# Kernel tuning notes

Hardware: AMD Instinct MI355X
Metric: run time of the kernel (lower is better)

## Reference

```python
import jax, jax.numpy as jnp
import numpy as np

B, S, D, H = 2, 2048, 2048, 16
DK = D // H


def setup_inputs() -> dict:
    key = jax.random.key(0)
    k1, k2, k3 = jax.random.split(key, 3)
    x = jax.random.normal(k1, (B, S, D), dtype=jnp.float32)
    # trunc-normal in the original; plain normal with matching std is fine for a numeric baseline
    std_qkv = 2.0 / (DK + D)  # note: original passes variance as std to trunc_normal_
    W_qkv = jax.random.normal(k2, (3 * D, D), dtype=jnp.float32) * std_qkv
    W_o = jax.random.normal(k3, (D, D), dtype=jnp.float32) * (1.0 / D)
    return {"x": x, "W_qkv": W_qkv, "W_o": W_o}


def reference(x, W_qkv, W_o):
    b, s, d = x.shape
    # fused QKV projection: y = x @ W_qkv^T
    qkv = jnp.einsum('bsd,ed->bse', x, W_qkv)  # [b, s, 3d]
    q, k, v = jnp.split(qkv, 3, axis=-1)
    # [b, s, d] -> [b, h, s, dk]
    def to_heads(t):
        return t.reshape(b, s, H, DK).transpose(0, 2, 1, 3)
    q, k, v = to_heads(q), to_heads(k), to_heads(v)
    scores = jnp.einsum('bhqd,bhkd->bhqk', q, k) / np.sqrt(DK).astype(np.float32)
    causal = jnp.tril(jnp.ones((s, s), dtype=bool))
    scores = jnp.where(causal, scores, -jnp.inf)
    att = jax.nn.softmax(scores, axis=-1)
    out = jnp.einsum('bhqk,bhkd->bhqd', att, v)  # [b, h, s, dk]
    out = out.transpose(0, 2, 1, 3).reshape(b, s, d)
    return jnp.einsum('bsd,od->bso', out, W_o)
```

## Files before the change

kernel.cpp:

```cpp
#include <hip/hip_runtime.h>

typedef _Float16 f16;
typedef _Float16 f16x4 __attribute__((ext_vector_type(4)));
typedef _Float16 f16x8 __attribute__((ext_vector_type(8)));
typedef float    f32x4 __attribute__((ext_vector_type(4)));

#define MFMA_F16(a,b,c) __builtin_amdgcn_mfma_f32_16x16x32_f16((a),(b),(c),0,0,0)

static constexpr int B_  = 2;
static constexpr int S_  = 2048;
static constexpr int D_  = 2048;
static constexpr int H_  = 16;
static constexpr int DK_ = 128;
static constexpr int K_  = 2048;

__device__ __forceinline__ void gload_lds16(const void* g, void* l) {
  __builtin_amdgcn_global_load_lds(
      (const __attribute__((address_space(1))) void*)g,
      (__attribute__((address_space(3))) void*)l, 16, 0, 0);
}

__global__ __launch_bounds__(256) void cast_all_kernel(const float* __restrict__ x,
                                                       const float* __restrict__ wqkv,
                                                       const float* __restrict__ wo,
                                                       f16* __restrict__ xb,
                                                       f16* __restrict__ wqkvb,
                                                       f16* __restrict__ wob) {
  const int total = 6291456;
  int i = blockIdx.x * 256 + threadIdx.x;
  int stride = gridDim.x * 256;
  for (int j = i; j < total; j += stride) {
    const float* src; f16* dst; int jj;
    if (j < 2097152)      { src = x;    dst = xb;    jj = j; }
    else if (j < 5242880) { src = wqkv; dst = wqkvb; jj = j - 2097152; }
    else                  { src = wo;   dst = wob;   jj = j - 5242880; }
    float4 v = reinterpret_cast<const float4*>(src)[jj];
    f16x4 o = {(f16)v.x, (f16)v.y, (f16)v.z, (f16)v.w};
    reinterpret_cast<f16x4*>(dst)[jj] = o;
  }
}


#define SYNCW0                                          \
  asm volatile("s_waitcnt vmcnt(0)" ::: "memory");      \
  __builtin_amdgcn_s_barrier();                         \
  asm volatile("" ::: "memory");

__device__ __forceinline__ void stage2(const f16* gA, const f16* gB, char* slot, int w) {
  gload_lds16(gA,      slot +         w * 1024);
  gload_lds16(gA + 32, slot +  8192 + w * 1024);
  gload_lds16(gB,      slot + 16384 + w * 1024);
  gload_lds16(gB + 32, slot + 24576 + w * 1024);
}

__device__ __forceinline__ void compute2(const char* slot, int aoff, int boff, int lro,
                                         f32x4 (&acc)[4][2]) {
  f16x8 a0[4], b0[2], a1[4], b1[2];
#pragma unroll
  for (int mi = 0; mi < 4; ++mi) {
    a0[mi] = *(const f16x8*)(slot +        aoff + mi * 1024 + lro);
    a1[mi] = *(const f16x8*)(slot + 8192 + aoff + mi * 1024 + lro);
  }
#pragma unroll
  for (int ni = 0; ni < 2; ++ni) {
    b0[ni] = *(const f16x8*)(slot + 16384 + boff + ni * 1024 + lro);
    b1[ni] = *(const f16x8*)(slot + 24576 + boff + ni * 1024 + lro);
  }
  __builtin_amdgcn_s_setprio(1);
#pragma unroll
  for (int mi = 0; mi < 4; ++mi)
#pragma unroll
    for (int ni = 0; ni < 2; ++ni)
      acc[mi][ni] = MFMA_F16(a0[mi], b0[ni], acc[mi][ni]);
#pragma unroll
  for (int mi = 0; mi < 4; ++mi)
#pragma unroll
    for (int ni = 0; ni < 2; ++ni)
      acc[mi][ni] = MFMA_F16(a1[mi], b1[ni], acc[mi][ni]);
  __builtin_amdgcn_s_setprio(0);
}

__device__ __forceinline__ void gemm_core_db(const f16* __restrict__ A,
                                             const f16* __restrict__ Bw,
                                             int brow, int bcol, char* lds,
                                             f32x4 (&acc)[4][2]) {
  const int tid = threadIdx.x;
  const int w = tid >> 6, l = tid & 63;
  const int lg = l >> 4, lr = l & 15;
  const int wm = w >> 2, wn = w & 3;
  const int lro = (lr * 4 + (lg ^ ((lr >> 1) & 3))) * 16;
  const int aoff = wm * 4096;
  const int boff = wn * 2048;

#pragma unroll
  for (int mi = 0; mi < 4; ++mi)
#pragma unroll
    for (int ni = 0; ni < 2; ++ni) acc[mi][ni] = (f32x4){0.f, 0.f, 0.f, 0.f};

  const int kgsrc = (l & 3) ^ ((l >> 3) & 3);
  const f16* gA = A  + (size_t)(brow * 128 + w * 16 + (l >> 2)) * K_ + kgsrc * 8;
  const f16* gB = Bw + (size_t)(bcol * 128 + w * 16 + (l >> 2)) * K_ + kgsrc * 8;

  char* s0 = lds;
  char* s1 = lds + 32768;

  stage2(gA, gB, s0, w);
  SYNCW0

  for (int tb = 0; tb < 16; ++tb) {
    const int t = tb * 2;
    stage2(gA + (size_t)(t + 1) * 64, gB + (size_t)(t + 1) * 64, s1, w);
    compute2(s0, aoff, boff, lro, acc);
    SYNCW0
    if (tb < 15)
      stage2(gA + (size_t)(t + 2) * 64, gB + (size_t)(t + 2) * 64, s0, w);
    compute2(s1, aoff, boff, lro, acc);
    SYNCW0
  }
}

__global__ __launch_bounds__(512, 4) void gemm_qkv_kernel(const f16* __restrict__ xb,
                                                          const f16* __restrict__ wqkv,
                                                          f16* __restrict__ Q,
                                                          f16* __restrict__ Kk,
                                                          f16* __restrict__ Vt) {
  __shared__ __align__(16) char lds[65536];
  const int bid = blockIdx.x;
  const int xcd = bid & 7;
  const int local = bid >> 3;
  const int brow = xcd * 4 + (local & 3);
  const int bcol = local >> 2;

  f32x4 acc[4][2];
  gemm_core_db(xb, wqkv, brow, bcol, lds, acc);

  const int tid = threadIdx.x;
  const int w = tid >> 6, l = tid & 63;
  const int lg = l >> 4, lr = l & 15;
  const int wm = w >> 2, wn = w & 3;

  const int which = bcol >> 4;
  const int h = bcol & 15;

  if (which == 2) {
#pragma unroll
    for (int mi = 0; mi < 4; ++mi) {
      const int m0 = brow * 128 + wm * 64 + mi * 16 + lg * 4;
      const int b = m0 >> 11, s = m0 & 2047;
#pragma unroll
      for (int ni = 0; ni < 2; ++ni) {
        const int dk = wn * 32 + ni * 16 + lr;
        f16x4 v = {(f16)acc[mi][ni][0], (f16)acc[mi][ni][1],
                   (f16)acc[mi][ni][2], (f16)acc[mi][ni][3]};
        *(f16x4*)(Vt + ((size_t)(b * H_ + h) * DK_ + dk) * S_ + s) = v;
      }
    }
  } else {
    f16* outp = (which == 0) ? Q : Kk;
    const float scale = (which == 0) ? 0.08838834764831845f : 1.0f;
#pragma unroll
    for (int mi = 0; mi < 4; ++mi) {
      const int m0 = brow * 128 + wm * 64 + mi * 16 + lg * 4;
#pragma unroll
      for (int ni = 0; ni < 2; ++ni) {
        const int dk = wn * 32 + ni * 16 + lr;
#pragma unroll
        for (int r = 0; r < 4; ++r) {
          const int mm = m0 + r;
          const int b = mm >> 11, s = mm & 2047;
          outp[(((size_t)b * H_ + h) * S_ + s) * DK_ + dk] = (f16)(acc[mi][ni][r] * scale);
        }
      }
    }
  }
}

__global__ __launch_bounds__(512, 4) void gemm_out_kernel(const f16* __restrict__ ab,
                                                          const f16* __restrict__ wo,
                                                          float* __restrict__ out) {
  __shared__ __align__(16) char lds[65536];
  const int bid = blockIdx.x;
  const int xcd = bid & 7;
  const int local = bid >> 3;
  const int brow = xcd * 4 + (local & 3);
  const int bcol = local >> 2;

  f32x4 acc[4][2];
  gemm_core_db(ab, wo, brow, bcol, lds, acc);

  const int tid = threadIdx.x;
  const int w = tid >> 6, l = tid & 63;
  const int lg = l >> 4, lr = l & 15;
  const int wm = w >> 2, wn = w & 3;

#pragma unroll
  for (int mi = 0; mi < 4; ++mi) {
    const int m0 = brow * 128 + wm * 64 + mi * 16 + lg * 4;
#pragma unroll
    for (int ni = 0; ni < 2; ++ni) {
      const int n = bcol * 128 + wn * 32 + ni * 16 + lr;
#pragma unroll
      for (int r = 0; r < 4; ++r)
        out[(size_t)(m0 + r) * D_ + n] = acc[mi][ni][r];
    }
  }
}

__global__ __launch_bounds__(256) void attn_kernel(const f16* __restrict__ Q,
                                                   const f16* __restrict__ Kg,
                                                   const f16* __restrict__ Vt,
                                                   f16* __restrict__ O) {
  __shared__ __align__(16) unsigned char Ks[64 * 256];
  __shared__ __align__(16) unsigned char Vs[128 * 128];
  __shared__ __align__(16) unsigned char Ps[4][16 * 128];

  const int bid = blockIdx.x;
  const int pr = bid & 15;
  const int h  = (bid >> 4) & 15;
  const int b  = bid >> 8;
  const int bh = b * H_ + h;
  const int tid = threadIdx.x;
  const int w = tid >> 6, l = tid & 63;
  const int lg = l >> 4, lr = l & 15;

  for (int half = 0; half < 2; ++half) {
    const int qt = half ? (31 - pr) : pr;

    const f16* Qg = Q + ((size_t)bh * S_ + qt * 64 + w * 16) * DK_;
    f16x8 qf[4];
#pragma unroll
    for (int kd = 0; kd < 4; ++kd)
      qf[kd] = *(const f16x8*)(Qg + (size_t)lr * DK_ + kd * 32 + lg * 8);

    f32x4 o[8];
#pragma unroll
    for (int n = 0; n < 8; ++n) o[n] = (f32x4){0.f, 0.f, 0.f, 0.f};
    float mrun[4] = {-1e30f, -1e30f, -1e30f, -1e30f};
    float lrun[4] = {0.f, 0.f, 0.f, 0.f};

    const int ntiles = qt + 1;
    for (int kt = 0; kt < ntiles; ++kt) {
      __syncthreads();
      const f16* Kt = Kg + ((size_t)bh * S_ + kt * 64) * DK_;
#pragma unroll
      for (int i = 0; i < 4; ++i) {
        const int chunk = i * 256 + tid;
        const int row = chunk >> 4, c8 = chunk & 15;
        uint4 v = *(const uint4*)(Kt + (size_t)row * DK_ + c8 * 8);
        *(uint4*)(Ks + row * 256 + ((c8 * 16) ^ ((row & 7) << 4))) = v;
      }
      const f16* Vtt = Vt + (size_t)bh * DK_ * S_ + kt * 64;
#pragma unroll
      for (int i = 0; i < 4; ++i) {
        const int chunk = i * 256 + tid;
        const int row = chunk >> 3, c8 = chunk & 7;
        uint4 v = *(const uint4*)(Vtt + (size_t)row * S_ + c8 * 8);
        *(uint4*)(Vs + row * 128 + ((c8 * 16) ^ ((row & 7) << 4))) = v;
      }
      __syncthreads();

      f32x4 s[4];
#pragma unroll
      for (int j = 0; j < 4; ++j) s[j] = (f32x4){0.f, 0.f, 0.f, 0.f};
      __builtin_amdgcn_s_setprio(1);
#pragma unroll
      for (int j = 0; j < 4; ++j) {
        const int row = j * 16 + lr;
#pragma unroll
        for (int kd = 0; kd < 4; ++kd) {
          f16x8 kf = *(const f16x8*)(Ks + row * 256 + ((kd * 64 + lg * 16) ^ ((row & 7) << 4)));
          s[j] = MFMA_F16(qf[kd], kf, s[j]);
        }
      }
      __builtin_amdgcn_s_setprio(0);
      if (kt == qt) {
#pragma unroll
        for (int j = 0; j < 4; ++j) {
          const int col = j * 16 + lr;
#pragma unroll
          for (int r = 0; r < 4; ++r) {
            const int qrow = w * 16 + lg * 4 + r;
            if (col > qrow) s[j][r] = -1e30f;
          }
        }
      }
      float scl[4];
#pragma unroll
      for (int r = 0; r < 4; ++r) {
        float m0 = fmaxf(fmaxf(s[0][r], s[1][r]), fmaxf(s[2][r], s[3][r]));
#pragma unroll
        for (int msk = 1; msk < 16; msk <<= 1) m0 = fmaxf(m0, __shfl_xor(m0, msk, 64));
        const float nm = fmaxf(mrun[r], m0);
        scl[r] = __expf(mrun[r] - nm);
        mrun[r] = nm;
      }
      float rs[4] = {0.f, 0.f, 0.f, 0.f};
#pragma unroll
      for (int j = 0; j < 4; ++j) {
#pragma unroll
        for (int r = 0; r < 4; ++r) {
          const float p = __expf(fmaxf(s[j][r] - mrun[r], -80.f));
          rs[r] += p;
          const int row = lg * 4 + r;
          const int cb = (j * 16 + lr) * 2;
          *(f16*)(Ps[w] + row * 128 + (cb ^ ((row & 7) << 4))) = (f16)p;
        }
      }
#pragma unroll
      for (int r = 0; r < 4; ++r) {
        float t = rs[r];
#pragma unroll
        for (int msk = 1; msk < 16; msk <<= 1) t += __shfl_xor(t, msk, 64);
        lrun[r] = lrun[r] * scl[r] + t;
      }
#pragma unroll
      for (int n = 0; n < 8; ++n)
#pragma unroll
        for (int r = 0; r < 4; ++r) o[n][r] *= scl[r];

      asm volatile("s_waitcnt lgkmcnt(0)" ::: "memory");

      __builtin_amdgcn_s_setprio(1);
#pragma unroll
      for (int ks = 0; ks < 2; ++ks) {
        f16x8 pf = *(const f16x8*)(Ps[w] + lr * 128 + ((ks * 64 + lg * 16) ^ ((lr & 7) << 4)));
#pragma unroll
        for (int n = 0; n < 8; ++n) {
          const int row = n * 16 + lr;
          f16x8 vf = *(const f16x8*)(Vs + row * 128 + ((ks * 64 + lg * 16) ^ ((row & 7) << 4)));
          o[n] = MFMA_F16(pf, vf, o[n]);
        }
      }
      __builtin_amdgcn_s_setprio(0);
    }

#pragma unroll
    for (int r = 0; r < 4; ++r) {
      const float inv = 1.0f / lrun[r];
      const int srow = qt * 64 + w * 16 + lg * 4 + r;
      f16* op = O + ((size_t)b * S_ + srow) * D_ + h * DK_;
#pragma unroll
      for (int n = 0; n < 8; ++n) op[n * 16 + lr] = (f16)(o[n][r] * inv);
    }
  }
}

extern "C" void kernel_launch(void* const* d_in, const int* in_sizes, int n_in,
                              void* d_out, int out_size, void* d_ws, size_t ws_size,
                              hipStream_t stream) {
  const float* x    = (const float*)d_in[0];
  const float* wqkv = (const float*)d_in[1];
  const float* wo   = (const float*)d_in[2];
  float* out = (float*)d_out;
  char* ws = (char*)d_ws;

  f16* xb     = (f16*)(ws + 0);
  f16* wqkvb  = (f16*)(ws + 16777216);
  f16* wob    = (f16*)(ws + 41943040);
  f16* Qb     = (f16*)(ws + 50331648);
  f16* Kb     = (f16*)(ws + 67108864);
  f16* Vtb    = (f16*)(ws + 83886080);
  f16* attn_o = (f16*)(ws + 0);

  cast_all_kernel<<<2048, 256, 0, stream>>>(x, wqkv, wo, xb, wqkvb, wob);

  gemm_qkv_kernel<<<1536, 512, 0, stream>>>(xb, wqkvb, Qb, Kb, Vtb);
  attn_kernel<<<512, 256, 0, stream>>>(Qb, Kb, Vtb, attn_o);
  gemm_out_kernel<<<512, 512, 0, stream>>>(attn_o, wob, out);
}
```

Before: 264.1 us.

## Double-buffer K/V tiles with async global-to-LDS loads in attention kernel

Replaces the synchronous register-staged K/V tile loads in the attention kernel with direct global_load_lds transfers into double-buffered LDS, prefetching the next tile while the current one is computed. LDS layout changes to 1KB sub-tile blocks with an XOR swizzle chosen so the MFMA fragment reads stay conflict-free. The point is to hide global memory latency behind the QK and PV MFMAs. In exchange LDS use roughly doubles, which may reduce occupancy, and correctness now relies on hand-placed vmcnt waits and barriers.

```diff
diff --git a/kernel.cpp b/kernel.cpp
--- a/kernel.cpp
+++ b/kernel.cpp
@@ -210,9 +210,9 @@
                                                    const f16* __restrict__ Kg,
                                                    const f16* __restrict__ Vt,
                                                    f16* __restrict__ O) {
-  __shared__ __align__(16) unsigned char Ks[64 * 256];
-  __shared__ __align__(16) unsigned char Vs[128 * 128];
-  __shared__ __align__(16) unsigned char Ps[4][16 * 128];
+  __shared__ __align__(16) char Kbuf2[2][16384];
+  __shared__ __align__(16) char Vbuf2[2][16384];
+  __shared__ __align__(16) unsigned char Ps[4][2048];
 
   const int bid = blockIdx.x;
   const int pr = bid & 15;
@@ -222,6 +222,12 @@
   const int tid = threadIdx.x;
   const int w = tid >> 6, l = tid & 63;
   const int lg = l >> 4, lr = l & 15;
+  const int lrow = l >> 2;
+  const int kgsrc = (l & 3) ^ ((l >> 3) & 3);
+  const int lro = (lr * 4 + (lg ^ ((lr >> 1) & 3))) * 16;
+
+  const f16* Kbase = Kg + (size_t)bh * S_ * DK_;
+  const f16* Vbase = Vt + (size_t)bh * DK_ * S_;
 
   for (int half = 0; half < 2; ++half) {
     const int qt = half ? (31 - pr) : pr;
@@ -239,25 +245,51 @@
     float lrun[4] = {0.f, 0.f, 0.f, 0.f};
 
     const int ntiles = qt + 1;
+
+    {
+      const f16* Kt = Kbase;
+      const f16* Vp = Vbase;
+#pragma unroll
+      for (int i = 0; i < 4; ++i) {
+        const int u = w * 4 + i;
+        gload_lds16(Kt + (size_t)((u >> 2) * 16 + lrow) * DK_ + (u & 3) * 32 + kgsrc * 8,
+                    Kbuf2[0] + u * 1024);
+      }
+#pragma unroll
+      for (int i = 0; i < 4; ++i) {
+        const int u = w * 4 + i;
+        gload_lds16(Vp + (size_t)((u >> 1) * 16 + lrow) * S_ + (u & 1) * 32 + kgsrc * 8,
+                    Vbuf2[0] + u * 1024);
+      }
+    }
+
     for (int kt = 0; kt < ntiles; ++kt) {
-      __syncthreads();
-      const f16* Kt = Kg + ((size_t)bh * S_ + kt * 64) * DK_;
-#pragma unroll
-      for (int i = 0; i < 4; ++i) {
-        const int chunk = i * 256 + tid;
-        const int row = chunk >> 4, c8 = chunk & 15;
-        uint4 v = *(const uint4*)(Kt + (size_t)row * DK_ + c8 * 8);
-        *(uint4*)(Ks + row * 256 + ((c8 * 16) ^ ((row & 7) << 4))) = v;
-      }
-      const f16* Vtt = Vt + (size_t)bh * DK_ * S_ + kt * 64;
-#pragma unroll
-      for (int i = 0; i < 4; ++i) {
-        const int chunk = i * 256 + tid;
-        const int row = chunk >> 3, c8 = chunk & 7;
-        uint4 v = *(const uint4*)(Vtt + (size_t)row * S_ + c8 * 8);
-        *(uint4*)(Vs + row * 128 + ((c8 * 16) ^ ((row & 7) << 4))) = v;
-      }
-      __syncthreads();
+      const int cur = kt & 1;
+      if (kt + 1 < ntiles) {
+        const f16* Kt = Kbase + (size_t)(kt + 1) * 64 * DK_;
+        const f16* Vp = Vbase + (kt + 1) * 64;
+        char* Kb = Kbuf2[cur ^ 1];
+        char* Vb = Vbuf2[cur ^ 1];
+#pragma unroll
+        for (int i = 0; i < 4; ++i) {
+          const int u = w * 4 + i;
+          gload_lds16(Kt + (size_t)((u >> 2) * 16 + lrow) * DK_ + (u & 3) * 32 + kgsrc * 8,
+                      Kb + u * 1024);
+        }
+#pragma unroll
+        for (int i = 0; i < 4; ++i) {
+          const int u = w * 4 + i;
+          gload_lds16(Vp + (size_t)((u >> 1) * 16 + lrow) * S_ + (u & 1) * 32 + kgsrc * 8,
+                      Vb + u * 1024);
+        }
+        asm volatile("s_waitcnt vmcnt(8)" ::: "memory");
+      } else {
+        asm volatile("s_waitcnt vmcnt(0)" ::: "memory");
+      }
+      __builtin_amdgcn_s_barrier();
+
+      const char* Kb = Kbuf2[cur];
+      const char* Vb = Vbuf2[cur];
 
       f32x4 s[4];
 #pragma unroll
@@ -265,10 +297,9 @@
       __builtin_amdgcn_s_setprio(1);
 #pragma unroll
       for (int j = 0; j < 4; ++j) {
-        const int row = j * 16 + lr;
 #pragma unroll
         for (int kd = 0; kd < 4; ++kd) {
-          f16x8 kf = *(const f16x8*)(Ks + row * 256 + ((kd * 64 + lg * 16) ^ ((row & 7) << 4)));
+          f16x8 kf = *(const f16x8*)(Kb + ((j << 2) + kd) * 1024 + lro);
           s[j] = MFMA_F16(qf[kd], kf, s[j]);
         }
       }
@@ -326,12 +357,12 @@
         f16x8 pf = *(const f16x8*)(Ps[w] + lr * 128 + ((ks * 64 + lg * 16) ^ ((lr & 7) << 4)));
 #pragma unroll
         for (int n = 0; n < 8; ++n) {
-          const int row = n * 16 + lr;
-          f16x8 vf = *(const f16x8*)(Vs + row * 128 + ((ks * 64 + lg * 16) ^ ((row & 7) << 4)));
+          f16x8 vf = *(const f16x8*)(Vb + ((n << 1) + ks) * 1024 + lro);
           o[n] = MFMA_F16(pf, vf, o[n]);
         }
       }
       __builtin_amdgcn_s_setprio(0);
+      __builtin_amdgcn_s_barrier();
     }
 
 #pragma unroll
```

New measurement: 266.9 us. About the same (+1.1%).

## Rewrite QKV GEMM with 128x256 tiles and triple-buffered K=32 pipeline

Applied to the files above, without the earlier changes.

Replaces the shared double-buffered QKV GEMM core with a dedicated kernel that uses 128x256 output tiles (each wave holds a 4x4 MFMA accumulator block) and halves the grid to 768 blocks. The K loop now stages 32-wide slices into three rotating LDS buffers and waits with a partial vmcnt, so more loads stay in flight across barriers. It also raises MFMA priority during compute. The larger tile is meant to improve operand reuse and cut global/LDS traffic per FLOP, at the cost of more registers, lower occupancy (the min-blocks launch bound is dropped) and fewer blocks to spread across CUs.

```diff
diff --git a/kernel.cpp b/kernel.cpp
--- a/kernel.cpp
+++ b/kernel.cpp
@@ -41,6 +41,126 @@
 }
 
 
+__device__ __forceinline__ void qkv_stage(const f16* pA, const f16* pB0, const f16* pB1,
+                                          int t, char* slot, int w) {
+  gload_lds16(pA  + t * 32, slot +         w * 1024);
+  gload_lds16(pB0 + t * 32, slot +  8192 + w * 1024);
+  gload_lds16(pB1 + t * 32, slot +  8192 + (w + 8) * 1024);
+}
+
+__device__ __forceinline__ void qkv_compute(const char* slot, int aoff, int boff, int lro,
+                                            f32x4 (&acc)[4][4]) {
+  f16x8 af[4], bf[4];
+#pragma unroll
+  for (int mi = 0; mi < 4; ++mi)
+    af[mi] = *(const f16x8*)(slot + aoff + mi * 1024 + lro);
+#pragma unroll
+  for (int ni = 0; ni < 4; ++ni)
+    bf[ni] = *(const f16x8*)(slot + 8192 + boff + ni * 1024 + lro);
+  __builtin_amdgcn_s_setprio(1);
+#pragma unroll
+  for (int mi = 0; mi < 4; ++mi)
+#pragma unroll
+    for (int ni = 0; ni < 4; ++ni)
+      acc[mi][ni] = MFMA_F16(af[mi], bf[ni], acc[mi][ni]);
+  __builtin_amdgcn_s_setprio(0);
+}
+
+#define QKV_SYNC(N)                                           \
+  asm volatile("s_waitcnt vmcnt(" #N ")" ::: "memory");       \
+  __builtin_amdgcn_s_barrier();                               \
+  asm volatile("" ::: "memory");
+
+__global__ __launch_bounds__(512) void gemm_qkv_kernel(const f16* __restrict__ xb,
+                                                       const f16* __restrict__ wqkv,
+                                                       f16* __restrict__ Q,
+                                                       f16* __restrict__ Kk,
+                                                       f16* __restrict__ Vt) {
+  __shared__ __align__(16) char lds[73728];
+  const int bid = blockIdx.x;
+  const int xcd = bid & 7;
+  const int local = bid >> 3;
+  const int brow = xcd * 4 + (local & 3);
+  const int bcol = local >> 2;
+
+  const int tid = threadIdx.x;
+  const int w = tid >> 6, l = tid & 63;
+  const int lg = l >> 4, lr = l & 15;
+  const int wm = w >> 2, wn = w & 3;
+  const int lro = (lr * 4 + (lg ^ ((lr >> 1) & 3))) * 16;
+  const int aoff = wm * 4096;
+  const int boff = wn * 4096;
+
+  f32x4 acc[4][4];
+#pragma unroll
+  for (int mi = 0; mi < 4; ++mi)
+#pragma unroll
+    for (int ni = 0; ni < 4; ++ni) acc[mi][ni] = (f32x4){0.f, 0.f, 0.f, 0.f};
+
+  const int lrow = l >> 2;
+  const int kgsrc = (l & 3) ^ ((l >> 3) & 3);
+  const f16* pA  = xb   + (size_t)(brow * 128 + w * 16 + lrow) * K_ + kgsrc * 8;
+  const f16* pB0 = wqkv + (size_t)(bcol * 256 + w * 16 + lrow) * K_ + kgsrc * 8;
+  const f16* pB1 = wqkv + (size_t)(bcol * 256 + (w + 8) * 16 + lrow) * K_ + kgsrc * 8;
+
+  char* s0 = lds;
+  char* s1 = lds + 24576;
+  char* s2 = lds + 49152;
+
+  qkv_stage(pA, pB0, pB1, 0, s0, w);
+  qkv_stage(pA, pB0, pB1, 1, s1, w);
+  QKV_SYNC(3)
+
+  for (int tb = 0; tb < 20; ++tb) {
+    const int t = 3 * tb;
+    qkv_stage(pA, pB0, pB1, t + 2, s2, w); qkv_compute(s0, aoff, boff, lro, acc); QKV_SYNC(3)
+    qkv_stage(pA, pB0, pB1, t + 3, s0, w); qkv_compute(s1, aoff, boff, lro, acc); QKV_SYNC(3)
+    qkv_stage(pA, pB0, pB1, t + 4, s1, w); qkv_compute(s2, aoff, boff, lro, acc); QKV_SYNC(3)
+  }
+  qkv_stage(pA, pB0, pB1, 62, s2, w); qkv_compute(s0, aoff, boff, lro, acc); QKV_SYNC(3)
+  qkv_stage(pA, pB0, pB1, 63, s0, w); qkv_compute(s1, aoff, boff, lro, acc); QKV_SYNC(3)
+  qkv_compute(s2, aoff, boff, lro, acc);
+  QKV_SYNC(0)
+  qkv_compute(s0, aoff, boff, lro, acc);
+
+  const int which = bcol >> 3;
+  const int nbase = (bcol & 7) * 256 + wn * 64;
+
+  if (which == 2) {
+#pragma unroll
+    for (int mi = 0; mi < 4; ++mi) {
+      const int m0 = brow * 128 + wm * 64 + mi * 16 + lg * 4;
+      const int b = m0 >> 11, s = m0 & 2047;
+#pragma unroll
+      for (int ni = 0; ni < 4; ++ni) {
+        const int n = nbase + ni * 16 + lr;
+        const int h = n >> 7, dk = n & 127;
+        f16x4 v = {(f16)acc[mi][ni][0], (f16)acc[mi][ni][1],
+                   (f16)acc[mi][ni][2], (f16)acc[mi][ni][3]};
+        *(f16x4*)(Vt + ((size_t)(b * H_ + h) * DK_ + dk) * S_ + s) = v;
+      }
+    }
+  } else {
+    f16* outp = (which == 0) ? Q : Kk;
+    const float scale = (which == 0) ? 0.08838834764831845f : 1.0f;
+#pragma unroll
+    for (int mi = 0; mi < 4; ++mi) {
+      const int m0 = brow * 128 + wm * 64 + mi * 16 + lg * 4;
+#pragma unroll
+      for (int ni = 0; ni < 4; ++ni) {
+        const int n = nbase + ni * 16 + lr;
+        const int h = n >> 7, dk = n & 127;
+#pragma unroll
+        for (int r = 0; r < 4; ++r) {
+          const int mm = m0 + r;
+          const int b = mm >> 11, s = mm & 2047;
+          outp[(((size_t)b * H_ + h) * S_ + s) * DK_ + dk] = (f16)(acc[mi][ni][r] * scale);
+        }
+      }
+    }
+  }
+}
+
 #define SYNCW0                                          \
   asm volatile("s_waitcnt vmcnt(0)" ::: "memory");      \
   __builtin_amdgcn_s_barrier();                         \
@@ -119,62 +239,6 @@
   }
 }
 
-__global__ __launch_bounds__(512, 4) void gemm_qkv_kernel(const f16* __restrict__ xb,
-                                                          const f16* __restrict__ wqkv,
-                                                          f16* __restrict__ Q,
-                                                          f16* __restrict__ Kk,
-                                                          f16* __restrict__ Vt) {
-  __shared__ __align__(16) char lds[65536];
-  const int bid = blockIdx.x;
-  const int xcd = bid & 7;
-  const int local = bid >> 3;
-  const int brow = xcd * 4 + (local & 3);
-  const int bcol = local >> 2;
-
-  f32x4 acc[4][2];
-  gemm_core_db(xb, wqkv, brow, bcol, lds, acc);
-
-  const int tid = threadIdx.x;
-  const int w = tid >> 6, l = tid & 63;
-  const int lg = l >> 4, lr = l & 15;
-  const int wm = w >> 2, wn = w & 3;
-
-  const int which = bcol >> 4;
-  const int h = bcol & 15;
-
-  if (which == 2) {
-#pragma unroll
-    for (int mi = 0; mi < 4; ++mi) {
-      const int m0 = brow * 128 + wm * 64 + mi * 16 + lg * 4;
-      const int b = m0 >> 11, s = m0 & 2047;
-#pragma unroll
-      for (int ni = 0; ni < 2; ++ni) {
-        const int dk = wn * 32 + ni * 16 + lr;
-        f16x4 v = {(f16)acc[mi][ni][0], (f16)acc[mi][ni][1],
-                   (f16)acc[mi][ni][2], (f16)acc[mi][ni][3]};
-        *(f16x4*)(Vt + ((size_t)(b * H_ + h) * DK_ + dk) * S_ + s) = v;
-      }
-    }
-  } else {
-    f16* outp = (which == 0) ? Q : Kk;
-    const float scale = (which == 0) ? 0.08838834764831845f : 1.0f;
-#pragma unroll
-    for (int mi = 0; mi < 4; ++mi) {
-      const int m0 = brow * 128 + wm * 64 + mi * 16 + lg * 4;
-#pragma unroll
-      for (int ni = 0; ni < 2; ++ni) {
-        const int dk = wn * 32 + ni * 16 + lr;
-#pragma unroll
-        for (int r = 0; r < 4; ++r) {
-          const int mm = m0 + r;
-          const int b = mm >> 11, s = mm & 2047;
-          outp[(((size_t)b * H_ + h) * S_ + s) * DK_ + dk] = (f16)(acc[mi][ni][r] * scale);
-        }
-      }
-    }
-  }
-}
-
 __global__ __launch_bounds__(512, 4) void gemm_out_kernel(const f16* __restrict__ ab,
                                                           const f16* __restrict__ wo,
                                                           float* __restrict__ out) {
@@ -364,7 +428,7 @@
 
   cast_all_kernel<<<2048, 256, 0, stream>>>(x, wqkv, wo, xb, wqkvb, wob);
 
-  gemm_qkv_kernel<<<1536, 512, 0, stream>>>(xb, wqkvb, Qb, Kb, Vtb);
+  gemm_qkv_kernel<<<768, 512, 0, stream>>>(xb, wqkvb, Qb, Kb, Vtb);
   attn_kernel<<<512, 256, 0, stream>>>(Qb, Kb, Vtb, attn_o);
   gemm_out_kernel<<<512, 512, 0, stream>>>(attn_o, wob, out);
 }
```

Result: slower. 270.0 us (+2.2%).

## Replace double-buffered GEMM k-loop with 4-slot ring and partial vmcnt waits

Applied to the files above, without the earlier changes.

The shared GEMM core used by the QKV and output projections now uses a four-slot LDS ring. Each slot holds one 32-wide k step, and loads are prefetched two steps ahead. Each barrier waits with vmcnt(2) instead of vmcnt(0), so the next tile's global-to-LDS loads stay in flight while the current tile is computed. This is meant to hide global load latency behind MFMA work. In exchange, the loop runs twice as many barriers with smaller compute chunks between them.

```diff
diff --git a/kernel.cpp b/kernel.cpp
--- a/kernel.cpp
+++ b/kernel.cpp
@@ -41,46 +41,37 @@
 }
 
 
-#define SYNCW0                                          \
-  asm volatile("s_waitcnt vmcnt(0)" ::: "memory");      \
-  __builtin_amdgcn_s_barrier();                         \
+__device__ __forceinline__ void stage_h(const f16* gA, const f16* gB, int h,
+                                        char* lds, int w) {
+  char* slot = lds + ((h & 3) << 14);
+  gload_lds16(gA + h * 32, slot +        w * 1024);
+  gload_lds16(gB + h * 32, slot + 8192 + w * 1024);
+}
+
+__device__ __forceinline__ void compute_h(const char* slot, int aoff, int boff, int lro,
+                                          f32x4 (&acc)[4][2]) {
+  f16x8 a[4], b[2];
+#pragma unroll
+  for (int mi = 0; mi < 4; ++mi)
+    a[mi] = *(const f16x8*)(slot + aoff + mi * 1024 + lro);
+#pragma unroll
+  for (int ni = 0; ni < 2; ++ni)
+    b[ni] = *(const f16x8*)(slot + 8192 + boff + ni * 1024 + lro);
+  __builtin_amdgcn_s_setprio(1);
+#pragma unroll
+  for (int mi = 0; mi < 4; ++mi)
+#pragma unroll
+    for (int ni = 0; ni < 2; ++ni)
+      acc[mi][ni] = MFMA_F16(a[mi], b[ni], acc[mi][ni]);
+  __builtin_amdgcn_s_setprio(0);
+}
+
+#define RSYNC(N)                                              \
+  asm volatile("s_waitcnt vmcnt(" #N ")" ::: "memory");       \
+  __builtin_amdgcn_s_barrier();                               \
   asm volatile("" ::: "memory");
 
-__device__ __forceinline__ void stage2(const f16* gA, const f16* gB, char* slot, int w) {
-  gload_lds16(gA,      slot +         w * 1024);
-  gload_lds16(gA + 32, slot +  8192 + w * 1024);
-  gload_lds16(gB,      slot + 16384 + w * 1024);
-  gload_lds16(gB + 32, slot + 24576 + w * 1024);
-}
-
-__device__ __forceinline__ void compute2(const char* slot, int aoff, int boff, int lro,
-                                         f32x4 (&acc)[4][2]) {
-  f16x8 a0[4], b0[2], a1[4], b1[2];
-#pragma unroll
-  for (int mi = 0; mi < 4; ++mi) {
-    a0[mi] = *(const f16x8*)(slot +        aoff + mi * 1024 + lro);
-    a1[mi] = *(const f16x8*)(slot + 8192 + aoff + mi * 1024 + lro);
-  }
-#pragma unroll
-  for (int ni = 0; ni < 2; ++ni) {
-    b0[ni] = *(const f16x8*)(slot + 16384 + boff + ni * 1024 + lro);
-    b1[ni] = *(const f16x8*)(slot + 24576 + boff + ni * 1024 + lro);
-  }
-  __builtin_amdgcn_s_setprio(1);
-#pragma unroll
-  for (int mi = 0; mi < 4; ++mi)
-#pragma unroll
-    for (int ni = 0; ni < 2; ++ni)
-      acc[mi][ni] = MFMA_F16(a0[mi], b0[ni], acc[mi][ni]);
-#pragma unroll
-  for (int mi = 0; mi < 4; ++mi)
-#pragma unroll
-    for (int ni = 0; ni < 2; ++ni)
-      acc[mi][ni] = MFMA_F16(a1[mi], b1[ni], acc[mi][ni]);
-  __builtin_amdgcn_s_setprio(0);
-}
-
-__device__ __forceinline__ void gemm_core_db(const f16* __restrict__ A,
+__device__ __forceinline__ void gemm_core_r4(const f16* __restrict__ A,
                                              const f16* __restrict__ Bw,
                                              int brow, int bcol, char* lds,
                                              f32x4 (&acc)[4][2]) {
@@ -101,22 +92,19 @@
   const f16* gA = A  + (size_t)(brow * 128 + w * 16 + (l >> 2)) * K_ + kgsrc * 8;
   const f16* gB = Bw + (size_t)(bcol * 128 + w * 16 + (l >> 2)) * K_ + kgsrc * 8;
 
-  char* s0 = lds;
-  char* s1 = lds + 32768;
-
-  stage2(gA, gB, s0, w);
-  SYNCW0
-
-  for (int tb = 0; tb < 16; ++tb) {
-    const int t = tb * 2;
-    stage2(gA + (size_t)(t + 1) * 64, gB + (size_t)(t + 1) * 64, s1, w);
-    compute2(s0, aoff, boff, lro, acc);
-    SYNCW0
-    if (tb < 15)
-      stage2(gA + (size_t)(t + 2) * 64, gB + (size_t)(t + 2) * 64, s0, w);
-    compute2(s1, aoff, boff, lro, acc);
-    SYNCW0
-  }
+  stage_h(gA, gB, 0, lds, w);
+  stage_h(gA, gB, 1, lds, w);
+  RSYNC(2)
+
+  for (int h = 0; h < 62; ++h) {
+    const char* slot = lds + ((h & 3) << 14);
+    compute_h(slot, aoff, boff, lro, acc);
+    stage_h(gA, gB, h + 2, lds, w);
+    RSYNC(2)
+  }
+  compute_h(lds + ((62 & 3) << 14), aoff, boff, lro, acc);
+  RSYNC(0)
+  compute_h(lds + ((63 & 3) << 14), aoff, boff, lro, acc);
 }
 
 __global__ __launch_bounds__(512, 4) void gemm_qkv_kernel(const f16* __restrict__ xb,
@@ -132,7 +120,7 @@
   const int bcol = local >> 2;
 
   f32x4 acc[4][2];
-  gemm_core_db(xb, wqkv, brow, bcol, lds, acc);
+  gemm_core_r4(xb, wqkv, brow, bcol, lds, acc);
 
   const int tid = threadIdx.x;
   const int w = tid >> 6, l = tid & 63;
@@ -186,7 +174,7 @@
   const int bcol = local >> 2;
 
   f32x4 acc[4][2];
-  gemm_core_db(ab, wo, brow, bcol, lds, acc);
+  gemm_core_r4(ab, wo, brow, bcol, lds, acc);
 
   const int tid = threadIdx.x;
   const int w = tid >> 6, l = tid & 63;
```

Result: slower. 289.8 us (+9.7%).
